# Optimization experiments

Measured on AMD Instinct MI355X. Metric: run time of the kernel, lower is better.

## Reference

```python
import jax, jax.numpy as jnp
import numpy as np
from functools import partial

KERNEL = (2, 2)  # kernel_size == stride in the module
HID = 128
OUT_F = 64


def setup_inputs() -> dict:
    key = jax.random.key(0)
    ks = jax.random.split(key, 7)
    s = 0.05
    return {
        "feats": jax.random.normal(ks[0], (32, 64, 256, 256), jnp.float32),
        "W_ih": jax.random.normal(ks[1], (4 * HID, 64), jnp.float32) * s,
        "W_hh": jax.random.normal(ks[2], (4 * HID, HID), jnp.float32) * s,
        "b_ih": jax.random.normal(ks[3], (4 * HID,), jnp.float32) * s,
        "b_hh": jax.random.normal(ks[4], (4 * HID,), jnp.float32) * s,
        "fc_w": jax.random.normal(ks[5], (OUT_F, HID), jnp.float32) * s,
        "fc_b": jax.random.normal(ks[6], (OUT_F,), jnp.float32) * s,
    }


def _lstm_conv(feats, W_ih, W_hh, b_ih, b_hh, fc_w, fc_b):
    N, C, H, W = feats.shape
    HH, WW = KERNEL
    DH, DW = KERNEL  # stride == kernel_size
    H_out = 1 + (H - HH) // DH
    W_out = 1 + (W - WW) // DW

    # torch nn.LSTM is seq-first: for field (N, HH*WW, C) the time axis is N and
    # the HH*WW patch pixels are independent batch sequences. h[:, -1, :] picks
    # the hidden trajectory of the LAST pixel of each patch, so only the
    # bottom-right pixel of every patch ever contributes to the output.
    x = jnp.transpose(feats, (0, 2, 3, 1))  # (N, H, W, C)
    rows = jnp.arange(H_out) * DH + (HH - 1)
    cols = jnp.arange(W_out) * DW + (WW - 1)
    xs = x[:, rows][:, :, cols]                  # (N, H_out, W_out, C)
    P = H_out * W_out
    xs = xs.reshape(N, P, C)                     # time N, batch P

    b = b_ih + b_hh
    # Precompute input projections for all time steps in one GEMM.
    gx = jnp.einsum('npc,gc->npg', xs, W_ih) + b  # (N, P, 4H)

    def step(carry, gx_t):
        h, c = carry
        gates = gx_t + h @ W_hh.T                 # (P, 4H)
        i, f, g, o = jnp.split(gates, 4, axis=-1)  # torch gate order i,f,g,o
        i = jax.nn.sigmoid(i)
        f = jax.nn.sigmoid(f)
        g = jnp.tanh(g)
        o = jax.nn.sigmoid(o)
        c = f * c + i * g
        h = o * jnp.tanh(c)
        return (h, c), h

    h0 = jnp.zeros((P, HID), feats.dtype)
    c0 = jnp.zeros((P, HID), feats.dtype)
    _, hs = jax.lax.scan(step, (h0, c0), gx)      # hs: (N, P, HID)

    out = jnp.einsum('nph,oh->nop', hs, fc_w) + fc_b[None, :, None]  # (N, OUT_F, P)
    return out.reshape(N, OUT_F, H_out, W_out)


def reference(feats, W_ih, W_hh, b_ih, b_hh, fc_w, fc_b):
    return _lstm_conv(feats, W_ih, W_hh, b_ih, b_hh, fc_w, fc_b)
```

## Files before the change

kernel.cpp:

```cpp
#include <hip/hip_runtime.h>
#include <stdint.h>


#define T_STEPS 32
#define C_IN    64
#define HID     128
#define OUT_F   64
#define BP      64
#define NBLK    256
#define NTHR    512

typedef __attribute__((ext_vector_type(8))) short short8_t;
typedef __attribute__((ext_vector_type(4))) short short4_t;
typedef __attribute__((ext_vector_type(4))) float float4_t;
typedef __attribute__((ext_vector_type(4))) unsigned int uint4_t;

#define L2E 1.44269504088896340736f

__device__ __forceinline__ short f2bf(float f) {
    uint32_t u = __builtin_bit_cast(uint32_t, f);
    u += 0x7fff + ((u >> 16) & 1);
    return (short)(u >> 16);
}
__device__ __forceinline__ uint32_t cvt_pk(float lo, float hi) {
    uint32_t r;
    asm("v_cvt_pk_bf16_f32 %0, %1, %2" : "=v"(r) : "v"(lo), "v"(hi));
    return r;
}
__device__ __forceinline__ float sig2(float a) {
    return __builtin_amdgcn_rcpf(1.0f + __builtin_amdgcn_exp2f(-a));
}
__device__ __forceinline__ float th2(float a) {
    return fmaf(-2.0f,
                __builtin_amdgcn_rcpf(1.0f + __builtin_amdgcn_exp2f(a)),
                1.0f);
}
__device__ __forceinline__ void barrier_lgkm() {
    asm volatile("s_waitcnt lgkmcnt(0)" ::: "memory");
    __builtin_amdgcn_s_barrier();
    asm volatile("" ::: "memory");
}

__global__ __launch_bounds__(NTHR, 2) void lstmconv_mfma(
    const float* __restrict__ feats,
    const float* __restrict__ W_ih,
    const float* __restrict__ W_hh,
    const float* __restrict__ b_ih,
    const float* __restrict__ b_hh,
    const float* __restrict__ fc_w,
    const float* __restrict__ fc_b,
    float* __restrict__ out)
{
    __shared__ __align__(16) short xB[2][8][512];
    __shared__ __align__(16) short hB[2][16][512];

    const int tid  = threadIdx.x;
    const int lane = tid & 63;
    const int wv   = tid >> 6;
    const int i16  = lane & 15;
    const int g4   = lane >> 4;
    const int p0   = blockIdx.x * BP;

    for (int i = tid; i < 2 * 16 * 512 / 2; i += NTHR)
        ((uint32_t*)hB)[i] = 0u;

    short8_t wfrag[4][6];
    float4_t bias_r[4];
    #pragma unroll
    for (int gi = 0; gi < 4; ++gi) {
        int row = 128 * gi + 16 * wv + i16;
        float sc = (gi == 2) ? 2.0f * L2E : L2E;
        #pragma unroll
        for (int kt = 0; kt < 6; ++kt) {
            int kk = 32 * kt + 8 * g4;
            const float* src = (kt < 2) ? &W_ih[row * C_IN + kk]
                                        : &W_hh[row * HID + (kk - 64)];
            short8_t f;
            #pragma unroll
            for (int e = 0; e < 8; ++e) f[e] = f2bf(src[e] * sc);
            wfrag[gi][kt] = f;
        }
        int g0 = 128 * gi + 16 * wv + 4 * g4;
        float4_t bi = *(const float4_t*)&b_ih[g0];
        float4_t bh = *(const float4_t*)&b_hh[g0];
        #pragma unroll
        for (int r = 0; r < 4; ++r) bias_r[gi][r] = (bi[r] + bh[r]) * sc;
    }

    const int m2  = wv & 3;
    const int nl  = wv >> 2;
    short8_t fcfrag[4];
    #pragma unroll
    for (int kt = 0; kt < 4; ++kt) {
        int kk = 32 * kt + 8 * g4;
        const float* src = &fc_w[(16 * m2 + i16) * HID + kk];
        short8_t f;
        #pragma unroll
        for (int e = 0; e < 8; ++e) f[e] = f2bf(src[e]);
        fcfrag[kt] = f;
    }
    const float4_t fcb = *(const float4_t*)&fc_b[16 * m2 + 4 * g4];

    const int prow  = 2 * (p0 >> 7) + 1;
    const int pcol0 = 2 * (p0 & 127) + 1;
    const int gbase = prow * 256 + pcol0 + 2 * lane;
    const int xtile = (wv >> 2) * 4 + (lane >> 4);
    const int xoff  = ((lane & 15) + 16 * (wv & 3)) * 8;
    const int htile_base = (wv >> 1) * 4;
    const int hoff  = (i16 + 16 * (2 * (wv & 1) + (g4 >> 1))) * 8 + 4 * (g4 & 1);

    {
        float g[8];
        #pragma unroll
        for (int e = 0; e < 8; ++e)
            g[e] = feats[((size_t)(8 * wv + e) << 16) + gbase];
        uint4_t pk = { cvt_pk(g[0], g[1]), cvt_pk(g[2], g[3]),
                       cvt_pk(g[4], g[5]), cvt_pk(g[6], g[7]) };
        *(uint4_t*)&xB[0][xtile][xoff] = pk;
    }

    float4_t accA[4][2], accB[4][2], cA[2], cB[2];
    #pragma unroll
    for (int nt = 0; nt < 2; ++nt) {
        cA[nt] = (float4_t){0.f, 0.f, 0.f, 0.f};
        cB[nt] = (float4_t){0.f, 0.f, 0.f, 0.f};
    }

    auto store_fc = [&](int tf, int chain, const float4_t& facc) {
        int ntg = chain * 2 + nl;
        #pragma unroll
        for (int r = 0; r < 4; ++r)
            out[((size_t)(tf * OUT_F + 16 * m2 + 4 * g4 + r) << 14)
                + p0 + 16 * ntg + i16] = facc[r];
    };

    auto do_fc = [&](int tf, int hb, int chain) {
        int ntg = chain * 2 + nl;
        float4_t facc = fcb;
        #pragma unroll
        for (int kt = 0; kt < 4; ++kt) {
            short8_t b = *(const short8_t*)&hB[hb][kt * 4 + ntg][lane * 8];
            facc = __builtin_amdgcn_mfma_f32_16x16x32_bf16(
                fcfrag[kt], b, facc, 0, 0, 0);
        }
        store_fc(tf, chain, facc);
    };

    auto gemm = [&](float4_t (&acc)[4][2], int xb, int hb, int chain,
                    float4_t& facc, bool fc_on) {
        #pragma unroll
        for (int gi = 0; gi < 4; ++gi)
            #pragma unroll
            for (int nt = 0; nt < 2; ++nt) acc[gi][nt] = bias_r[gi];
        #pragma unroll
        for (int nt = 0; nt < 2; ++nt) {
            int ntg = chain * 2 + nt;
            short8_t bf[6];
            #pragma unroll
            for (int kt = 0; kt < 6; ++kt) {
                const short* src = (kt < 2) ? &xB[xb][kt * 4 + ntg][0]
                                            : &hB[hb][(kt - 2) * 4 + ntg][0];
                bf[kt] = *(const short8_t*)&src[lane * 8];
            }
            #pragma unroll
            for (int kt = 0; kt < 6; ++kt)
                #pragma unroll
                for (int gi = 0; gi < 4; ++gi)
                    acc[gi][nt] = __builtin_amdgcn_mfma_f32_16x16x32_bf16(
                        wfrag[gi][kt], bf[kt], acc[gi][nt], 0, 0, 0);
            if (fc_on && nt == nl) {
                #pragma unroll
                for (int kt = 2; kt < 6; ++kt)
                    facc = __builtin_amdgcn_mfma_f32_16x16x32_bf16(
                        fcfrag[kt - 2], bf[kt], facc, 0, 0, 0);
            }
        }
    };

    auto cell = [&](float4_t (&acc)[4][2], float4_t (&c)[2], int hb, int chain) {
        #pragma unroll
        for (int nt = 0; nt < 2; ++nt) {
            float4_t cv = c[nt];
            float hv[4];
            #pragma unroll
            for (int r = 0; r < 4; ++r) {
                float ig = sig2(acc[0][nt][r]);
                float fg = sig2(acc[1][nt][r]);
                float cand = th2(acc[2][nt][r]);
                float og = sig2(acc[3][nt][r]);
                float cn = fmaf(fg, cv[r], ig * cand);
                cv[r] = cn;
                hv[r] = og * th2(cn * (2.0f * L2E));
            }
            c[nt] = cv;
            uint32_t h0 = cvt_pk(hv[0], hv[1]);
            uint32_t h1 = cvt_pk(hv[2], hv[3]);
            uint32_t* dst = (uint32_t*)&hB[hb][htile_base + chain * 2 + nt][hoff];
            dst[0] = h0; dst[1] = h1;
        }
    };

    __syncthreads();

    #pragma unroll 1
    for (int t = 0; t < T_STEPS; ++t) {
        const int cur = t & 1;
        const int nxt = cur ^ 1;

        float g[8];
        if (t < T_STEPS - 1) {
            #pragma unroll
            for (int e = 0; e < 8; ++e)
                g[e] = feats[((size_t)((t + 1) * C_IN + 8 * wv + e) << 16) + gbase];
        }
        float4_t faccA = fcb;
        gemm(accA, cur, nxt, 0, faccA, t > 0);
        if (t > 0) store_fc(t - 1, 0, faccA);
        if (t > 0) cell(accB, cB, nxt, 1);

        barrier_lgkm();

        float4_t faccB = fcb;
        gemm(accB, cur, nxt, 1, faccB, t > 0);
        if (t > 0) store_fc(t - 1, 1, faccB);
        cell(accA, cA, cur, 0);

        if (t < T_STEPS - 1) {
            uint4_t pk = { cvt_pk(g[0], g[1]), cvt_pk(g[2], g[3]),
                           cvt_pk(g[4], g[5]), cvt_pk(g[6], g[7]) };
            *(uint4_t*)&xB[nxt][xtile][xoff] = pk;
        }

        barrier_lgkm();
    }

    cell(accB, cB, 1, 1);
    __syncthreads();
    do_fc(T_STEPS - 1, 1, 0);
    do_fc(T_STEPS - 1, 1, 1);
}

extern "C" void kernel_launch(void* const* d_in, const int* in_sizes, int n_in,
                              void* d_out, int out_size, void* d_ws, size_t ws_size,
                              hipStream_t stream) {
    const float* feats = (const float*)d_in[0];
    const float* W_ih  = (const float*)d_in[1];
    const float* W_hh  = (const float*)d_in[2];
    const float* b_ih  = (const float*)d_in[3];
    const float* b_hh  = (const float*)d_in[4];
    const float* fc_w  = (const float*)d_in[5];
    const float* fc_b  = (const float*)d_in[6];
    float* out = (float*)d_out;

    lstmconv_mfma<<<NBLK, NTHR, 0, stream>>>(feats, W_ih, W_hh, b_ih, b_hh,
                                             fc_w, fc_b, out);
}
```

Before: 157.2 us.

## Merge staggered two-chain LSTM step into single-barrier batched GEMM then cells

```diff
diff --git a/kernel.cpp b/kernel.cpp
--- a/kernel.cpp
+++ b/kernel.cpp
@@ -148,32 +148,34 @@
 
     auto gemm = [&](float4_t (&acc)[4][2], int xb, int hb, int chain,
                     float4_t& facc, bool fc_on) {
-        #pragma unroll
-        for (int gi = 0; gi < 4; ++gi)
-            #pragma unroll
-            for (int nt = 0; nt < 2; ++nt) acc[gi][nt] = bias_r[gi];
+        short8_t bf[2][6];
         #pragma unroll
         for (int nt = 0; nt < 2; ++nt) {
             int ntg = chain * 2 + nt;
-            short8_t bf[6];
             #pragma unroll
             for (int kt = 0; kt < 6; ++kt) {
                 const short* src = (kt < 2) ? &xB[xb][kt * 4 + ntg][0]
                                             : &hB[hb][(kt - 2) * 4 + ntg][0];
-                bf[kt] = *(const short8_t*)&src[lane * 8];
+                bf[nt][kt] = *(const short8_t*)&src[lane * 8];
             }
-            #pragma unroll
-            for (int kt = 0; kt < 6; ++kt)
+        }
+        #pragma unroll
+        for (int gi = 0; gi < 4; ++gi)
+            #pragma unroll
+            for (int nt = 0; nt < 2; ++nt) acc[gi][nt] = bias_r[gi];
+        #pragma unroll
+        for (int kt = 0; kt < 6; ++kt)
+            #pragma unroll
+            for (int nt = 0; nt < 2; ++nt)
                 #pragma unroll
                 for (int gi = 0; gi < 4; ++gi)
                     acc[gi][nt] = __builtin_amdgcn_mfma_f32_16x16x32_bf16(
-                        wfrag[gi][kt], bf[kt], acc[gi][nt], 0, 0, 0);
-            if (fc_on && nt == nl) {
-                #pragma unroll
-                for (int kt = 2; kt < 6; ++kt)
-                    facc = __builtin_amdgcn_mfma_f32_16x16x32_bf16(
-                        fcfrag[kt - 2], bf[kt], facc, 0, 0, 0);
-            }
+                        wfrag[gi][kt], bf[nt][kt], acc[gi][nt], 0, 0, 0);
+        if (fc_on) {
+            #pragma unroll
+            for (int kt = 2; kt < 6; ++kt)
+                facc = __builtin_amdgcn_mfma_f32_16x16x32_bf16(
+                    fcfrag[kt - 2], bf[nl][kt], facc, 0, 0, 0);
         }
     };
 
@@ -213,17 +215,18 @@
             for (int e = 0; e < 8; ++e)
                 g[e] = feats[((size_t)((t + 1) * C_IN + 8 * wv + e) << 16) + gbase];
         }
-        float4_t faccA = fcb;
-        gemm(accA, cur, nxt, 0, faccA, t > 0);
-        if (t > 0) store_fc(t - 1, 0, faccA);
-        if (t > 0) cell(accB, cB, nxt, 1);
-
-        barrier_lgkm();
-
-        float4_t faccB = fcb;
-        gemm(accB, cur, nxt, 1, faccB, t > 0);
-        if (t > 0) store_fc(t - 1, 1, faccB);
-        cell(accA, cA, cur, 0);
+
+        float4_t faccA = fcb, faccB = fcb;
+        gemm(accA, cur, cur, 0, faccA, t > 0);
+        gemm(accB, cur, cur, 1, faccB, t > 0);
+
+        cell(accA, cA, nxt, 0);
+        cell(accB, cB, nxt, 1);
+
+        if (t > 0) {
+            store_fc(t - 1, 0, faccA);
+            store_fc(t - 1, 1, faccB);
+        }
 
         if (t < T_STEPS - 1) {
             uint4_t pk = { cvt_pk(g[0], g[1]), cvt_pk(g[2], g[3]),
@@ -234,10 +237,8 @@
         barrier_lgkm();
     }
 
-    cell(accB, cB, 1, 1);
-    __syncthreads();
-    do_fc(T_STEPS - 1, 1, 0);
-    do_fc(T_STEPS - 1, 1, 1);
+    do_fc(T_STEPS - 1, 0, 0);
+    do_fc(T_STEPS - 1, 0, 1);
 }
 
 extern "C" void kernel_launch(void* const* d_in, const int* in_sizes, int n_in,
```

After: 478.8 us. 205% more time.
